# Optimization experiments

Hardware: AMD Instinct MI355X
Metric: run time of the kernel (lower is better)

The kernel has to match this reference:

```python
import jax, jax.numpy as jnp
import numpy as np

B, CQ, CVK, L, H = 4, 256, 256, 2048, 8
D = CVK // H  # depth per head = 32
EPS = 1e-5    # BatchNorm eps


def setup_inputs() -> dict:
    key = jax.random.key(0)
    ks = jax.random.split(key, 32)
    n = lambda i, s, sc=1.0: jax.random.normal(ks[i], s, dtype=jnp.float32) * sc
    u = lambda i, s: jax.random.uniform(ks[i], s, dtype=jnp.float32, minval=0.5, maxval=1.5)
    inp = {
        'v': n(0, (B, CVK, L)), 'k': n(1, (B, CVK, L)), 'q': n(2, (B, CQ, L)),
        # trainable positional encodings (pe_q: image_shape_q, pe_vk: image_shape_vk)
        'pe_q': n(3, (CQ, L)), 'pe_vk': n(4, (CVK, L)),
        # W_query / W_key / W_value: Conv1d(kernel=1) weight [out,in] + bias, then BatchNorm1d (eval mode)
        'wq': n(5, (CVK, CQ), 0.05), 'bq': n(6, (CVK,), 0.05),
        'gq': 1.0 + n(7, (CVK,), 0.1), 'betaq': n(8, (CVK,), 0.1), 'mq': n(9, (CVK,), 0.1), 'varq': u(10, (CVK,)),
        'wk': n(11, (CVK, CVK), 0.05), 'bk': n(12, (CVK,), 0.05),
        'gk': 1.0 + n(13, (CVK,), 0.1), 'betak': n(14, (CVK,), 0.1), 'mk': n(15, (CVK,), 0.1), 'vark': u(16, (CVK,)),
        'wv': n(17, (CVK, CVK), 0.05), 'bv': n(18, (CVK,), 0.05),
        'gv': 1.0 + n(19, (CVK,), 0.1), 'betav': n(20, (CVK,), 0.1), 'mv': n(21, (CVK,), 0.1), 'varv': u(22, (CVK,)),
        # out_proj (zero-init in original; randomized here so gradients are non-trivial)
        'wo': n(23, (CQ, CVK), 0.05), 'bo': n(24, (CQ,), 0.05),
    }
    return inp


def _conv1(x, w, b):  # 1x1 conv == channel matmul: [b,c,l] -> [b,o,l]
    return jnp.einsum('oc,bcl->bol', w, x) + b[None, :, None]


def _bn(x, g, beta, mean, var):  # eval-mode BatchNorm1d over channel dim
    scale = g / jnp.sqrt(var + EPS)
    return (x - mean[:, None]) * scale[:, None] + beta[:, None]


def _mha(v, k, q, pe_q, pe_vk, wq, bq, gq, betaq, mq, varq,
         wk, bk, gk, betak, mk, vark, wv, bv, gv, betav, mv, varv, wo, bo):
    q_orig = q
    b = q.shape[0]
    vv = v + pe_vk[None]
    kk = k + pe_vk[None]
    qq = q + pe_q[None]
    qp = _bn(_conv1(qq, wq, bq), gq, betaq, mq, varq)   # [b, CVK, L]
    kp = _bn(_conv1(kk, wk, bk), gk, betak, mk, vark)
    vp = _bn(_conv1(vv, wv, bv), gv, betav, mv, varv)
    # split heads: [b, H, D, L]
    qh = qp.reshape(b, H, D, -1)
    kh = kp.reshape(b, H, D, -1)
    vh = vp.reshape(b, H, D, -1)
    # scaled dot-product attention over sequence dim (l: query pos, m: key pos)
    scores = jnp.einsum('bhdl,bhdm->bhlm', qh, kh) / jnp.sqrt(jnp.float32(D))
    p = jax.nn.softmax(scores, axis=-1)
    a = jnp.einsum('bhlm,bhdm->bhdl', p, vh)            # [b, H, D, L]
    a = a.reshape(b, H * D, -1)                          # [b, CVK, L]
    out = _conv1(a, wo, bo)                              # [b, CQ, L]
    return q_orig + out


def reference(v, k, q, pe_q, pe_vk, wq, bq, gq, betaq, mq, varq,
              wk, bk, gk, betak, mk, vark, wv, bv, gv, betav, mv, varv, wo, bo):
    return _mha(v, k, q, pe_q, pe_vk, wq, bq, gq, betaq, mq, varq,
                wk, bk, gk, betak, mk, vark, wv, bv, gv, betav, mv, varv, wo, bo)
```

## Files before the change

kernel.cpp:

```cpp
#include <hip/hip_runtime.h>
#include <hip/hip_bf16.h>

#define BB 4
#define CC 256
#define LL 2048
#define HH 8
#define DD 32
#define EPSV 1e-5f

typedef __bf16 bf16x8 __attribute__((ext_vector_type(8)));
typedef __bf16 bf16x4 __attribute__((ext_vector_type(4)));
typedef __bf16 bf16x2 __attribute__((ext_vector_type(2)));
typedef float  f32x4  __attribute__((ext_vector_type(4)));
typedef float  f32x16 __attribute__((ext_vector_type(16)));
typedef unsigned int u32x4 __attribute__((ext_vector_type(4)));

static __device__ __forceinline__ unsigned pkbf(float lo, float hi) {
    bf16x2 p; p[0] = (__bf16)lo; p[1] = (__bf16)hi;
    return __builtin_bit_cast(unsigned, p);
}

__global__ __launch_bounds__(256) void wprep_kernel(
    const float* __restrict__ wq, const float* __restrict__ bq,
    const float* __restrict__ gq, const float* __restrict__ betaq,
    const float* __restrict__ mq, const float* __restrict__ varq,
    const float* __restrict__ wk, const float* __restrict__ bk,
    const float* __restrict__ gk, const float* __restrict__ betak,
    const float* __restrict__ mk, const float* __restrict__ vark,
    const float* __restrict__ wv, const float* __restrict__ bv,
    const float* __restrict__ gv, const float* __restrict__ betav,
    const float* __restrict__ mv, const float* __restrict__ varv,
    const float* __restrict__ wo,
    __bf16* __restrict__ wqb, __bf16* __restrict__ wkb,
    __bf16* __restrict__ wvb, __bf16* __restrict__ wob,
    float* __restrict__ bqf, float* __restrict__ bkf, float* __restrict__ bvf,
    float qscale)
{
    const int which = blockIdx.y;
    const float* w    = which==0?wq:(which==1?wk:(which==2?wv:wo));
    const float* bias = which==0?bq:(which==1?bk:bv);
    const float* g    = which==0?gq:(which==1?gk:gv);
    const float* beta = which==0?betaq:(which==1?betak:betav);
    const float* mean = which==0?mq:(which==1?mk:mv);
    const float* var  = which==0?varq:(which==1?vark:varv);
    __bf16* wout = which==0?wqb:(which==1?wkb:(which==2?wvb:wob));
    float*  bout = which==0?bqf:(which==1?bkf:bvf);
    const float extra = (which==0) ? qscale : 1.0f;

    const int t = threadIdx.x;
    const int base = blockIdx.x * 4096;
    for (int i = 0; i < 16; ++i) {
        const int idx = base + i * 256 + t;
        const int o = idx >> 8;
        const float sc = (which < 3) ? (g[o] * rsqrtf(var[o] + EPSV) * extra) : 1.0f;
        wout[idx] = (__bf16)(w[idx] * sc);
    }
    if (blockIdx.x == 0 && which < 3) {
        const int o = t;
        const float sc = g[o] * rsqrtf(var[o] + EPSV);
        bout[o] = ((bias[o] - mean[o]) * sc + beta[o]) * extra;
    }
}

__global__ __launch_bounds__(256) void xprep_kernel(
    const float* __restrict__ qin, const float* __restrict__ kin,
    const float* __restrict__ vin, const float* __restrict__ peq,
    const float* __restrict__ pevk,
    __bf16* __restrict__ xq, __bf16* __restrict__ xk, __bf16* __restrict__ xv)
{
    __shared__ __align__(16) float xs[64][66];
    const int lt = blockIdx.x * 64;
    const int ct = blockIdx.y * 64;
    const int z  = blockIdx.z;
    const int b  = z & 3;
    const int which = z >> 2;
    const int t  = threadIdx.x;

    const float* xin = which == 0 ? qin : (which == 1 ? kin : vin);
    const float* pe  = which == 0 ? peq : pevk;
    __bf16* xout     = which == 0 ? xq  : (which == 1 ? xk : xv);

    for (int i = 0; i < 8; ++i) {
        const int idx = i * 256 + t;
        const int row = idx >> 5;
        const int lch = idx & 31;
        const float2 xv2 = *(const float2*)&xin[(size_t)(b * CC + ct + row) * LL + lt + lch * 2];
        const float2 pv2 = *(const float2*)&pe[(size_t)(ct + row) * LL + lt + lch * 2];
        float2 s; s.x = xv2.x + pv2.x; s.y = xv2.y + pv2.y;
        *(float2*)&xs[row][lch * 2] = s;
    }
    __syncthreads();

    for (int i = 0; i < 2; ++i) {
        const int idx = i * 256 + t;
        const int lrow = idx >> 3;
        const int ch   = idx & 7;
        bf16x8 v;
        #pragma unroll
        for (int j = 0; j < 8; ++j) v[j] = (__bf16)xs[ch * 8 + j][lrow];
        *(bf16x8*)&xout[(size_t)(b * LL + lt + lrow) * CC + ct + ch * 8] = v;
    }
}

__global__ __launch_bounds__(512) void qkv_gemm_kernel(
    const __bf16* __restrict__ wqb, const __bf16* __restrict__ wkb,
    const __bf16* __restrict__ wvb,
    const __bf16* __restrict__ xq, const __bf16* __restrict__ xk,
    const __bf16* __restrict__ xv,
    const float* __restrict__ bqf, const float* __restrict__ bkf,
    const float* __restrict__ bvf,
    __bf16* __restrict__ qTo, __bf16* __restrict__ kTo, __bf16* __restrict__ vNo)
{
    __shared__ __align__(16) __bf16 Wl[64][136];
    __shared__ __align__(16) __bf16 Xl[128][136];
    __bf16 (*Tl)[72] = (__bf16(*)[72])Xl;

    const int z = blockIdx.z;
    const int which = z >> 2;
    const int b = z & 3;
    const __bf16* W    = which==0 ? wqb : (which==1 ? wkb : wvb);
    const __bf16* X    = which==0 ? xq  : (which==1 ? xk  : xv);
    const float*  bias = which==0 ? bqf : (which==1 ? bkf : bvf);

    const int lt = blockIdx.x * 128;
    const int ot = blockIdx.y * 64;
    const int t  = threadIdx.x;
    const int wv = t >> 6;
    const int wm = wv >> 2;
    const int wn = wv & 3;
    const int l  = t & 63;
    const int lq = l & 15;
    const int g  = l >> 4;

    f32x4 acc[2][2];
    #pragma unroll
    for (int mi = 0; mi < 2; ++mi)
        #pragma unroll
        for (int ni = 0; ni < 2; ++ni) acc[mi][ni] = (f32x4){0.f,0.f,0.f,0.f};

    for (int ks = 0; ks < 2; ++ks) {
        __syncthreads();
        #pragma unroll
        for (int i = 0; i < 2; ++i) {
            const int idx = i * 512 + t;
            const int row = idx >> 4, ch = idx & 15;
            *(bf16x8*)&Wl[row][ch * 8] =
                *(const bf16x8*)&W[(size_t)(ot + row) * CC + ks * 128 + ch * 8];
        }
        #pragma unroll
        for (int i = 0; i < 4; ++i) {
            const int idx = i * 512 + t;
            const int row = idx >> 4, ch = idx & 15;
            *(bf16x8*)&Xl[row][ch * 8] =
                *(const bf16x8*)&X[(size_t)(b * LL + lt + row) * CC + ks * 128 + ch * 8];
        }
        __syncthreads();

        #pragma unroll
        for (int kk = 0; kk < 4; ++kk) {
            bf16x8 af[2], bfr[2];
            #pragma unroll
            for (int mi = 0; mi < 2; ++mi)
                af[mi] = *(const bf16x8*)&Wl[wm * 32 + mi * 16 + lq][kk * 32 + g * 8];
            #pragma unroll
            for (int ni = 0; ni < 2; ++ni)
                bfr[ni] = *(const bf16x8*)&Xl[wn * 32 + ni * 16 + lq][kk * 32 + g * 8];
            #pragma unroll
            for (int mi = 0; mi < 2; ++mi)
                #pragma unroll
                for (int ni = 0; ni < 2; ++ni)
                    acc[mi][ni] = __builtin_amdgcn_mfma_f32_16x16x32_bf16(
                        af[mi], bfr[ni], acc[mi][ni], 0, 0, 0);
        }
    }

    if (which < 2) {
        __bf16* outT = which==0 ? qTo : kTo;
        __syncthreads();
        #pragma unroll
        for (int mi = 0; mi < 2; ++mi) {
            const float4 b4 = *(const float4*)&bias[ot + wm * 32 + mi * 16 + g * 4];
            #pragma unroll
            for (int ni = 0; ni < 2; ++ni) {
                bf16x4 pv;
                pv[0] = (__bf16)(acc[mi][ni][0] + b4.x);
                pv[1] = (__bf16)(acc[mi][ni][1] + b4.y);
                pv[2] = (__bf16)(acc[mi][ni][2] + b4.z);
                pv[3] = (__bf16)(acc[mi][ni][3] + b4.w);
                *(bf16x4*)&Tl[wn * 32 + ni * 16 + lq][wm * 32 + mi * 16 + g * 4] = pv;
            }
        }
        __syncthreads();
        #pragma unroll
        for (int i = 0; i < 2; ++i) {
            const int idx = i * 512 + t;
            const int lrow = idx >> 3, ch = idx & 7;
            *(bf16x8*)&outT[(size_t)(b * LL + lt + lrow) * CC + ot + ch * 8] =
                *(const bf16x8*)&Tl[lrow][ch * 8];
        }
    } else {
        #pragma unroll
        for (int mi = 0; mi < 2; ++mi) {
            const float4 b4 = *(const float4*)&bias[ot + wm * 32 + mi * 16 + g * 4];
            const float bb[4] = {b4.x, b4.y, b4.z, b4.w};
            #pragma unroll
            for (int ni = 0; ni < 2; ++ni) {
                const int col = lt + wn * 32 + ni * 16 + lq;
                #pragma unroll
                for (int r = 0; r < 4; ++r) {
                    const int o = ot + wm * 32 + mi * 16 + g * 4 + r;
                    vNo[(size_t)(b * CC + o) * LL + col] = (__bf16)(acc[mi][ni][r] + bb[r]);
                }
            }
        }
    }
}

__global__ __launch_bounds__(256) void attn_mfma_kernel(
    const __bf16* __restrict__ qT, const __bf16* __restrict__ kT,
    const __bf16* __restrict__ vN, __bf16* __restrict__ aT)
{
    __shared__ __align__(16) __bf16 KB[64 * 32];
    __shared__ __align__(16) __bf16 VB[32 * 64];

    const int qb = blockIdx.x;
    const int h  = blockIdx.y;
    const int b  = blockIdx.z;
    const int t  = threadIdx.x;
    const int w  = t >> 6;
    const int l  = t & 63;
    const int lq = l & 31;
    const int hi = l >> 5;

    const int q0 = qb * 128 + w * 32;

    const __bf16* qrow = qT + ((size_t)(b * LL) + q0 + lq) * CC + h * DD;
    const bf16x8 qf0 = *(const bf16x8*)&qrow[hi * 8];
    const bf16x8 qf1 = *(const bf16x8*)&qrow[16 + hi * 8];

    const __bf16* kTb = kT + (size_t)(b * LL) * CC + h * DD;
    const __bf16* vNb = vN + ((size_t)(b * CC) + h * DD) * LL;

    const int skey = t >> 2, spart = t & 3;
    const int sd   = t >> 3, sp    = t & 7;
    const int kwi  = skey * 32 + (spart ^ ((skey >> 1) & 3)) * 8;
    const int vwi  = sd * 64 + (sp ^ (sd & 7)) * 8;

    bf16x8 kreg = *(const bf16x8*)&kTb[(size_t)skey * CC + spart * 8];
    bf16x8 vreg = *(const bf16x8*)&vNb[(size_t)sd * LL + sp * 8];

    f32x16 O;
    #pragma unroll
    for (int r = 0; r < 16; ++r) O[r] = 0.f;
    float ssum = 0.f;

    for (int kt0 = 0; kt0 < LL; kt0 += 64) {
        __syncthreads();
        *(bf16x8*)&KB[kwi] = kreg;
        *(bf16x8*)&VB[vwi] = vreg;
        __syncthreads();
        if (kt0 + 64 < LL) {
            kreg = *(const bf16x8*)&kTb[(size_t)(kt0 + 64 + skey) * CC + spart * 8];
            vreg = *(const bf16x8*)&vNb[(size_t)sd * LL + (kt0 + 64) + sp * 8];
        }

        #pragma unroll
        for (int kb = 0; kb < 64; kb += 32) {
            const int key = kb + lq;
            f32x16 S;
            #pragma unroll
            for (int r = 0; r < 16; ++r) S[r] = 0.f;
            {
                const bf16x8 kf0 = *(const bf16x8*)&KB[key * 32 + ((hi    ) ^ ((key >> 1) & 3)) * 8];
                S = __builtin_amdgcn_mfma_f32_32x32x16_bf16(kf0, qf0, S, 0, 0, 0);
                const bf16x8 kf1 = *(const bf16x8*)&KB[key * 32 + ((2 + hi) ^ ((key >> 1) & 3)) * 8];
                S = __builtin_amdgcn_mfma_f32_32x32x16_bf16(kf1, qf1, S, 0, 0, 0);
            }
            float e[16];
            #pragma unroll
            for (int r = 0; r < 16; ++r) e[r] = __builtin_amdgcn_exp2f(S[r]);
            float s = 0.f;
            #pragma unroll
            for (int r = 0; r < 16; r += 4) s += (e[r] + e[r+1]) + (e[r+2] + e[r+3]);
            ssum += s;
            unsigned a[8];
            #pragma unroll
            for (int i = 0; i < 8; ++i) a[i] = pkbf(e[2*i], e[2*i+1]);
            #pragma unroll
            for (int c = 0; c < 2; ++c) {
                unsigned w0 = a[4*c+0], w1 = a[4*c+1], w2 = a[4*c+2], w3 = a[4*c+3];
                asm volatile("v_permlane32_swap_b32 %0, %1" : "+v"(w0), "+v"(w2));
                asm volatile("v_permlane32_swap_b32 %0, %1" : "+v"(w1), "+v"(w3));
                u32x4 pv4 = {w0, w1, w2, w3};
                const bf16x8 pf = __builtin_bit_cast(bf16x8, pv4);
                const int slot = (kb >> 3) + 2 * c + hi;
                const bf16x8 vf = *(const bf16x8*)&VB[lq * 64 + (slot ^ (lq & 7)) * 8];
                O = __builtin_amdgcn_mfma_f32_32x32x16_bf16(vf, pf, O, 0, 0, 0);
            }
        }
    }

    ssum += __shfl_xor(ssum, 32);
    const float inv = 1.f / ssum;

    __bf16* arow = aT + ((size_t)(b * LL) + q0 + lq) * CC + h * DD;
    #pragma unroll
    for (int gi = 0; gi < 4; ++gi) {
        bf16x4 ov;
        #pragma unroll
        for (int r = 0; r < 4; ++r) ov[r] = (__bf16)(O[4*gi + r] * inv);
        *(bf16x4*)&arow[8 * gi + 4 * hi] = ov;
    }
}

__global__ __launch_bounds__(512) void outproj_kernel(
    const __bf16* __restrict__ W, const __bf16* __restrict__ X,
    const float* __restrict__ bias, const float* __restrict__ resid,
    float* __restrict__ outF)
{
    __shared__ __align__(16) __bf16 Wl[64][136];
    __shared__ __align__(16) __bf16 Xl[128][136];

    const int lt = blockIdx.x * 128;
    const int ot = blockIdx.y * 64;
    const int b  = blockIdx.z;
    const int t  = threadIdx.x;
    const int wv = t >> 6;
    const int wm = wv >> 2;
    const int wn = wv & 3;
    const int l  = t & 63;
    const int lq = l & 15;
    const int g  = l >> 4;

    f32x4 acc[2][2];
    #pragma unroll
    for (int mi = 0; mi < 2; ++mi)
        #pragma unroll
        for (int ni = 0; ni < 2; ++ni) acc[mi][ni] = (f32x4){0.f,0.f,0.f,0.f};

    for (int ks = 0; ks < 2; ++ks) {
        __syncthreads();
        #pragma unroll
        for (int i = 0; i < 2; ++i) {
            const int idx = i * 512 + t;
            const int row = idx >> 4, ch = idx & 15;
            *(bf16x8*)&Wl[row][ch * 8] =
                *(const bf16x8*)&W[(size_t)(ot + row) * CC + ks * 128 + ch * 8];
        }
        #pragma unroll
        for (int i = 0; i < 4; ++i) {
            const int idx = i * 512 + t;
            const int row = idx >> 4, ch = idx & 15;
            *(bf16x8*)&Xl[row][ch * 8] =
                *(const bf16x8*)&X[(size_t)(b * LL + lt + row) * CC + ks * 128 + ch * 8];
        }
        __syncthreads();

        #pragma unroll
        for (int kk = 0; kk < 4; ++kk) {
            bf16x8 af[2], bfr[2];
            #pragma unroll
            for (int mi = 0; mi < 2; ++mi)
                af[mi] = *(const bf16x8*)&Wl[wm * 32 + mi * 16 + lq][kk * 32 + g * 8];
            #pragma unroll
            for (int ni = 0; ni < 2; ++ni)
                bfr[ni] = *(const bf16x8*)&Xl[wn * 32 + ni * 16 + lq][kk * 32 + g * 8];
            #pragma unroll
            for (int mi = 0; mi < 2; ++mi)
                #pragma unroll
                for (int ni = 0; ni < 2; ++ni)
                    acc[mi][ni] = __builtin_amdgcn_mfma_f32_16x16x32_bf16(
                        af[mi], bfr[ni], acc[mi][ni], 0, 0, 0);
        }
    }

    #pragma unroll
    for (int mi = 0; mi < 2; ++mi) {
        const float4 b4 = *(const float4*)&bias[ot + wm * 32 + mi * 16 + g * 4];
        const float bb[4] = {b4.x, b4.y, b4.z, b4.w};
        #pragma unroll
        for (int ni = 0; ni < 2; ++ni) {
            const int col = lt + wn * 32 + ni * 16 + lq;
            #pragma unroll
            for (int r = 0; r < 4; ++r) {
                const int o = ot + wm * 32 + mi * 16 + g * 4 + r;
                const size_t a = (size_t)(b * CC + o) * LL + col;
                outF[a] = acc[mi][ni][r] + bb[r] + resid[a];
            }
        }
    }
}

extern "C" void kernel_launch(void* const* d_in, const int* in_sizes, int n_in,
                              void* d_out, int out_size, void* d_ws, size_t ws_size,
                              hipStream_t stream)
{
    const float* v     = (const float*)d_in[0];
    const float* k     = (const float*)d_in[1];
    const float* q     = (const float*)d_in[2];
    const float* pe_q  = (const float*)d_in[3];
    const float* pe_vk = (const float*)d_in[4];
    const float* wq    = (const float*)d_in[5];
    const float* bq    = (const float*)d_in[6];
    const float* gq    = (const float*)d_in[7];
    const float* betaq = (const float*)d_in[8];
    const float* mq    = (const float*)d_in[9];
    const float* varq  = (const float*)d_in[10];
    const float* wk    = (const float*)d_in[11];
    const float* bk    = (const float*)d_in[12];
    const float* gk    = (const float*)d_in[13];
    const float* betak = (const float*)d_in[14];
    const float* mk    = (const float*)d_in[15];
    const float* vark  = (const float*)d_in[16];
    const float* wv    = (const float*)d_in[17];
    const float* bv    = (const float*)d_in[18];
    const float* gv    = (const float*)d_in[19];
    const float* betav = (const float*)d_in[20];
    const float* mv    = (const float*)d_in[21];
    const float* varv  = (const float*)d_in[22];
    const float* wo    = (const float*)d_in[23];
    const float* bo    = (const float*)d_in[24];

    float* out = (float*)d_out;

    const size_t E = (size_t)BB * CC * LL;
    __bf16* xq  = (__bf16*)d_ws;
    __bf16* xk  = xq + E;
    __bf16* xv  = xk + E;
    __bf16* qT  = xv + E;
    __bf16* kT  = qT + E;
    __bf16* vN  = kT + E;
    __bf16* aT  = vN + E;
    __bf16* wqb = aT + E;
    __bf16* wkb = wqb + 65536;
    __bf16* wvb = wkb + 65536;
    __bf16* wob = wvb + 65536;
    float*  bqf = (float*)(wob + 65536);
    float*  bkf = bqf + 256;
    float*  bvf = bkf + 256;

    const float qscale = 0.17677669529663687f * 1.4426950408889634f;

    hipLaunchKernelGGL(wprep_kernel, dim3(16, 4), dim3(256), 0, stream,
                       wq, bq, gq, betaq, mq, varq,
                       wk, bk, gk, betak, mk, vark,
                       wv, bv, gv, betav, mv, varv,
                       wo, wqb, wkb, wvb, wob, bqf, bkf, bvf, qscale);

    hipLaunchKernelGGL(xprep_kernel, dim3(32, 4, 12), dim3(256), 0, stream,
                       q, k, v, pe_q, pe_vk, xq, xk, xv);

    hipLaunchKernelGGL(qkv_gemm_kernel, dim3(16, 4, 12), dim3(512), 0, stream,
                       wqb, wkb, wvb, xq, xk, xv, bqf, bkf, bvf, qT, kT, vN);

    hipLaunchKernelGGL(attn_mfma_kernel, dim3(16, HH, BB), dim3(256), 0, stream,
                       qT, kT, vN, aT);

    hipLaunchKernelGGL(outproj_kernel, dim3(16, 4, 4), dim3(512), 0, stream,
                       wob, aT, bo, q, out);
}
```

Before: 70.69 us.

## Merge prep kernels, double-buffer attention K/V tiles, shrink outproj tiles

Folds the weight-prep kernel into the activation-prep kernel as an extra z-slice, which saves one launch. The attention kernel now stages 128-key K/V tiles into double-buffered LDS with a register prefetch two tiles ahead, so there is one barrier per 128 keys instead of two per 64. It also wraps the MFMAs in s_setprio. The out-projection moves to 256-thread blocks with 64x64 tiles, doubling its grid to 512 blocks. These changes raise LDS use in the attention kernel and add more blocks to outproj.

```diff
diff --git a/kernel.cpp b/kernel.cpp
--- a/kernel.cpp
+++ b/kernel.cpp
@@ -20,7 +20,11 @@
     return __builtin_bit_cast(unsigned, p);
 }
 
-__global__ __launch_bounds__(256) void wprep_kernel(
+__global__ __launch_bounds__(256) void prep_kernel(
+    const float* __restrict__ qin, const float* __restrict__ kin,
+    const float* __restrict__ vin, const float* __restrict__ peq,
+    const float* __restrict__ pevk,
+    __bf16* __restrict__ xq, __bf16* __restrict__ xk, __bf16* __restrict__ xv,
     const float* __restrict__ wq, const float* __restrict__ bq,
     const float* __restrict__ gq, const float* __restrict__ betaq,
     const float* __restrict__ mq, const float* __restrict__ varq,
@@ -36,45 +40,41 @@
     float* __restrict__ bqf, float* __restrict__ bkf, float* __restrict__ bvf,
     float qscale)
 {
-    const int which = blockIdx.y;
-    const float* w    = which==0?wq:(which==1?wk:(which==2?wv:wo));
-    const float* bias = which==0?bq:(which==1?bk:bv);
-    const float* g    = which==0?gq:(which==1?gk:gv);
-    const float* beta = which==0?betaq:(which==1?betak:betav);
-    const float* mean = which==0?mq:(which==1?mk:mv);
-    const float* var  = which==0?varq:(which==1?vark:varv);
-    __bf16* wout = which==0?wqb:(which==1?wkb:(which==2?wvb:wob));
-    float*  bout = which==0?bqf:(which==1?bkf:bvf);
-    const float extra = (which==0) ? qscale : 1.0f;
-
+    __shared__ __align__(16) float xs[64][66];
     const int t = threadIdx.x;
-    const int base = blockIdx.x * 4096;
-    for (int i = 0; i < 16; ++i) {
-        const int idx = base + i * 256 + t;
-        const int o = idx >> 8;
-        const float sc = (which < 3) ? (g[o] * rsqrtf(var[o] + EPSV) * extra) : 1.0f;
-        wout[idx] = (__bf16)(w[idx] * sc);
-    }
-    if (blockIdx.x == 0 && which < 3) {
-        const int o = t;
-        const float sc = g[o] * rsqrtf(var[o] + EPSV);
-        bout[o] = ((bias[o] - mean[o]) * sc + beta[o]) * extra;
-    }
-}
-
-__global__ __launch_bounds__(256) void xprep_kernel(
-    const float* __restrict__ qin, const float* __restrict__ kin,
-    const float* __restrict__ vin, const float* __restrict__ peq,
-    const float* __restrict__ pevk,
-    __bf16* __restrict__ xq, __bf16* __restrict__ xk, __bf16* __restrict__ xv)
-{
-    __shared__ __align__(16) float xs[64][66];
+
+    if (blockIdx.z == 12) {
+        const int which = blockIdx.y;
+        const float* w    = which==0?wq:(which==1?wk:(which==2?wv:wo));
+        const float* bias = which==0?bq:(which==1?bk:bv);
+        const float* g    = which==0?gq:(which==1?gk:gv);
+        const float* beta = which==0?betaq:(which==1?betak:betav);
+        const float* mean = which==0?mq:(which==1?mk:mv);
+        const float* var  = which==0?varq:(which==1?vark:varv);
+        __bf16* wout = which==0?wqb:(which==1?wkb:(which==2?wvb:wob));
+        float*  bout = which==0?bqf:(which==1?bkf:bvf);
+        const float extra = (which==0) ? qscale : 1.0f;
+
+        const int base = blockIdx.x * 2048;
+        for (int i = 0; i < 8; ++i) {
+            const int idx = base + i * 256 + t;
+            const int o = idx >> 8;
+            const float sc = (which < 3) ? (g[o] * rsqrtf(var[o] + EPSV) * extra) : 1.0f;
+            wout[idx] = (__bf16)(w[idx] * sc);
+        }
+        if (blockIdx.x == 0 && which < 3) {
+            const int o = t;
+            const float sc = g[o] * rsqrtf(var[o] + EPSV);
+            bout[o] = ((bias[o] - mean[o]) * sc + beta[o]) * extra;
+        }
+        return;
+    }
+
     const int lt = blockIdx.x * 64;
     const int ct = blockIdx.y * 64;
     const int z  = blockIdx.z;
     const int b  = z & 3;
     const int which = z >> 2;
-    const int t  = threadIdx.x;
 
     const float* xin = which == 0 ? qin : (which == 1 ? kin : vin);
     const float* pe  = which == 0 ? peq : pevk;
@@ -220,8 +220,8 @@
     const __bf16* __restrict__ qT, const __bf16* __restrict__ kT,
     const __bf16* __restrict__ vN, __bf16* __restrict__ aT)
 {
-    __shared__ __align__(16) __bf16 KB[64 * 32];
-    __shared__ __align__(16) __bf16 VB[32 * 64];
+    __shared__ __align__(16) __bf16 KB[2][128 * 32];
+    __shared__ __align__(16) __bf16 VB[2][32 * 128];
 
     const int qb = blockIdx.x;
     const int h  = blockIdx.y;
@@ -241,40 +241,56 @@
     const __bf16* kTb = kT + (size_t)(b * LL) * CC + h * DD;
     const __bf16* vNb = vN + ((size_t)(b * CC) + h * DD) * LL;
 
-    const int skey = t >> 2, spart = t & 3;
-    const int sd   = t >> 3, sp    = t & 7;
-    const int kwi  = skey * 32 + (spart ^ ((skey >> 1) & 3)) * 8;
-    const int vwi  = sd * 64 + (sp ^ (sd & 7)) * 8;
-
-    bf16x8 kreg = *(const bf16x8*)&kTb[(size_t)skey * CC + spart * 8];
-    bf16x8 vreg = *(const bf16x8*)&vNb[(size_t)sd * LL + sp * 8];
+    const int s0 = t, s1 = 256 + t;
+    const int sk0 = s0 >> 2, sp0 = s0 & 3;
+    const int sk1 = s1 >> 2, sp1 = s1 & 3;
+    const int sd0 = s0 >> 4, sv0 = s0 & 15;
+    const int sd1 = s1 >> 4, sv1 = s1 & 15;
+    const int kw0 = sk0 * 32 + (sp0 ^ ((sk0 >> 1) & 3)) * 8;
+    const int kw1 = sk1 * 32 + (sp1 ^ ((sk1 >> 1) & 3)) * 8;
+    const int vw0 = sd0 * 128 + (sv0 ^ (sd0 & 7)) * 8;
+    const int vw1 = sd1 * 128 + (sv1 ^ (sd1 & 7)) * 8;
+
+    bf16x8 kr0, kr1, vr0, vr1;
+    #define LOADREGS(KT0) \
+        kr0 = *(const bf16x8*)&kTb[(size_t)((KT0) + sk0) * CC + sp0 * 8]; \
+        kr1 = *(const bf16x8*)&kTb[(size_t)((KT0) + sk1) * CC + sp1 * 8]; \
+        vr0 = *(const bf16x8*)&vNb[(size_t)sd0 * LL + (KT0) + sv0 * 8];   \
+        vr1 = *(const bf16x8*)&vNb[(size_t)sd1 * LL + (KT0) + sv1 * 8];
+    #define WRITEBUF(BUF) \
+        *(bf16x8*)&KB[BUF][kw0] = kr0; *(bf16x8*)&KB[BUF][kw1] = kr1; \
+        *(bf16x8*)&VB[BUF][vw0] = vr0; *(bf16x8*)&VB[BUF][vw1] = vr1;
+
+    LOADREGS(0)
+    WRITEBUF(0)
+    LOADREGS(128)
 
     f32x16 O;
     #pragma unroll
     for (int r = 0; r < 16; ++r) O[r] = 0.f;
     float ssum = 0.f;
 
-    for (int kt0 = 0; kt0 < LL; kt0 += 64) {
-        __syncthreads();
-        *(bf16x8*)&KB[kwi] = kreg;
-        *(bf16x8*)&VB[vwi] = vreg;
-        __syncthreads();
-        if (kt0 + 64 < LL) {
-            kreg = *(const bf16x8*)&kTb[(size_t)(kt0 + 64 + skey) * CC + spart * 8];
-            vreg = *(const bf16x8*)&vNb[(size_t)sd * LL + (kt0 + 64) + sp * 8];
-        }
-
-        #pragma unroll
-        for (int kb = 0; kb < 64; kb += 32) {
+    const int NT = LL / 128;
+    for (int it = 0; it < NT; ++it) {
+        const int buf = it & 1;
+        __syncthreads();
+        const __bf16* KBb = KB[buf];
+        const __bf16* VBb = VB[buf];
+
+        #pragma unroll
+        for (int kb = 0; kb < 128; kb += 32) {
             const int key = kb + lq;
+            const int ksw = (key >> 1) & 3;
             f32x16 S;
             #pragma unroll
             for (int r = 0; r < 16; ++r) S[r] = 0.f;
             {
-                const bf16x8 kf0 = *(const bf16x8*)&KB[key * 32 + ((hi    ) ^ ((key >> 1) & 3)) * 8];
+                const bf16x8 kf0 = *(const bf16x8*)&KBb[key * 32 + ((hi    ) ^ ksw) * 8];
+                const bf16x8 kf1 = *(const bf16x8*)&KBb[key * 32 + ((2 + hi) ^ ksw) * 8];
+                __builtin_amdgcn_s_setprio(1);
                 S = __builtin_amdgcn_mfma_f32_32x32x16_bf16(kf0, qf0, S, 0, 0, 0);
-                const bf16x8 kf1 = *(const bf16x8*)&KB[key * 32 + ((2 + hi) ^ ((key >> 1) & 3)) * 8];
                 S = __builtin_amdgcn_mfma_f32_32x32x16_bf16(kf1, qf1, S, 0, 0, 0);
+                __builtin_amdgcn_s_setprio(0);
             }
             float e[16];
             #pragma unroll
@@ -294,11 +310,18 @@
                 u32x4 pv4 = {w0, w1, w2, w3};
                 const bf16x8 pf = __builtin_bit_cast(bf16x8, pv4);
                 const int slot = (kb >> 3) + 2 * c + hi;
-                const bf16x8 vf = *(const bf16x8*)&VB[lq * 64 + (slot ^ (lq & 7)) * 8];
+                const bf16x8 vf = *(const bf16x8*)&VBb[lq * 128 + (slot ^ (lq & 7)) * 8];
+                __builtin_amdgcn_s_setprio(1);
                 O = __builtin_amdgcn_mfma_f32_32x32x16_bf16(vf, pf, O, 0, 0, 0);
+                __builtin_amdgcn_s_setprio(0);
             }
         }
-    }
+
+        if (it + 1 < NT) { WRITEBUF(buf ^ 1) }
+        if (it + 2 < NT) { LOADREGS((it + 2) * 128) }
+    }
+    #undef LOADREGS
+    #undef WRITEBUF
 
     ssum += __shfl_xor(ssum, 32);
     const float inv = 1.f / ssum;
@@ -313,21 +336,21 @@
     }
 }
 
-__global__ __launch_bounds__(512) void outproj_kernel(
+__global__ __launch_bounds__(256) void outproj_kernel(
     const __bf16* __restrict__ W, const __bf16* __restrict__ X,
     const float* __restrict__ bias, const float* __restrict__ resid,
     float* __restrict__ outF)
 {
     __shared__ __align__(16) __bf16 Wl[64][136];
-    __shared__ __align__(16) __bf16 Xl[128][136];
-
-    const int lt = blockIdx.x * 128;
+    __shared__ __align__(16) __bf16 Xl[64][136];
+
+    const int lt = blockIdx.x * 64;
     const int ot = blockIdx.y * 64;
     const int b  = blockIdx.z;
     const int t  = threadIdx.x;
     const int wv = t >> 6;
-    const int wm = wv >> 2;
-    const int wn = wv & 3;
+    const int wm = wv >> 1;
+    const int wn = wv & 1;
     const int l  = t & 63;
     const int lq = l & 15;
     const int g  = l >> 4;
@@ -341,15 +364,15 @@
     for (int ks = 0; ks < 2; ++ks) {
         __syncthreads();
         #pragma unroll
-        for (int i = 0; i < 2; ++i) {
-            const int idx = i * 512 + t;
+        for (int i = 0; i < 4; ++i) {
+            const int idx = i * 256 + t;
             const int row = idx >> 4, ch = idx & 15;
             *(bf16x8*)&Wl[row][ch * 8] =
                 *(const bf16x8*)&W[(size_t)(ot + row) * CC + ks * 128 + ch * 8];
         }
         #pragma unroll
         for (int i = 0; i < 4; ++i) {
-            const int idx = i * 512 + t;
+            const int idx = i * 256 + t;
             const int row = idx >> 4, ch = idx & 15;
             *(bf16x8*)&Xl[row][ch * 8] =
                 *(const bf16x8*)&X[(size_t)(b * LL + lt + row) * CC + ks * 128 + ch * 8];
@@ -441,21 +464,19 @@
 
     const float qscale = 0.17677669529663687f * 1.4426950408889634f;
 
-    hipLaunchKernelGGL(wprep_kernel, dim3(16, 4), dim3(256), 0, stream,
+    hipLaunchKernelGGL(prep_kernel, dim3(32, 4, 13), dim3(256), 0, stream,
+                       q, k, v, pe_q, pe_vk, xq, xk, xv,
                        wq, bq, gq, betaq, mq, varq,
                        wk, bk, gk, betak, mk, vark,
                        wv, bv, gv, betav, mv, varv,
                        wo, wqb, wkb, wvb, wob, bqf, bkf, bvf, qscale);
 
-    hipLaunchKernelGGL(xprep_kernel, dim3(32, 4, 12), dim3(256), 0, stream,
-                       q, k, v, pe_q, pe_vk, xq, xk, xv);
-
     hipLaunchKernelGGL(qkv_gemm_kernel, dim3(16, 4, 12), dim3(512), 0, stream,
                        wqb, wkb, wvb, xq, xk, xv, bqf, bkf, bvf, qT, kT, vN);
 
     hipLaunchKernelGGL(attn_mfma_kernel, dim3(16, HH, BB), dim3(256), 0, stream,
                        qT, kT, vN, aT);
 
-    hipLaunchKernelGGL(outproj_kernel, dim3(16, 4, 4), dim3(512), 0, stream,
+    hipLaunchKernelGGL(outproj_kernel, dim3(32, 4, 4), dim3(256), 0, stream,
                        wob, aT, bo, q, out);
 }
```

Result: faster. 65.38 us (-7.5%).
